# Optimization experiments

Hardware: AMD Instinct MI355X
Metric: run time of the kernel (lower is better)

The kernel has to match this reference:

```python
import jax, jax.numpy as jnp
import numpy as np

B, S, D = 4, 1024, 1024
H, DK, DV = 16, 64, 64
LN_EPS = 1e-5

def setup_inputs() -> dict:
    key = jax.random.key(0)
    ks = jax.random.split(key, 8)
    sc_q = 1.0 / np.sqrt(D)
    return {
        "Q": jax.random.normal(ks[0], (B, S, D), jnp.float32),
        "K": jax.random.normal(ks[1], (B, S, D), jnp.float32),
        "V": jax.random.normal(ks[2], (B, S, D), jnp.float32),
        "mask": jnp.zeros((B, S, S), dtype=bool),
        "W_Q": jax.random.normal(ks[3], (D, H * DK), jnp.float32) * sc_q,
        "W_K": jax.random.normal(ks[4], (D, H * DK), jnp.float32) * sc_q,
        "W_V": jax.random.normal(ks[5], (D, H * DV), jnp.float32) * sc_q,
        "W_O": jax.random.normal(ks[6], (H * DV, D), jnp.float32) * (1.0 / np.sqrt(H * DV)),
        "ln_gamma": jnp.ones((D,), jnp.float32),
        "ln_beta": jnp.zeros((D,), jnp.float32),
    }

def reference(Q, K, V, mask, W_Q, W_K, W_V, W_O, ln_gamma, ln_beta):
    residual = Q
    # projections -> [B, H, S, dk/dv]
    q = (Q @ W_Q).reshape(B, S, H, DK).transpose(0, 2, 1, 3)
    k = (K @ W_K).reshape(B, S, H, DK).transpose(0, 2, 1, 3)
    v = (V @ W_V).reshape(B, S, H, DV).transpose(0, 2, 1, 3)
    # scores [B, H, Sq, Sk]
    scores = jnp.einsum('bhqd,bhkd->bhqk', q, k) / jnp.sqrt(jnp.float32(DK))
    scores = jnp.where(mask[:, None, :, :], -jnp.inf, scores)
    # faithful to original: softmax over dim=2 (the QUERY axis)
    attn = jax.nn.softmax(scores, axis=2)
    out = jnp.einsum('bhqk,bhkd->bhqd', attn, v)  # [B, H, Sq, dv]
    out = out.transpose(0, 2, 1, 3).reshape(B, S, H * DV)
    out = out @ W_O + residual
    # LayerNorm over last dim
    mu = jnp.mean(out, axis=-1, keepdims=True)
    var = jnp.var(out, axis=-1, keepdims=True)
    out = (out - mu) * jax.lax.rsqrt(var + LN_EPS) * ln_gamma + ln_beta
    return out, attn
```

## Files before the change

### kernel.cpp

```cpp
#include <hip/hip_runtime.h>
#include <hip/hip_bf16.h>


typedef __bf16 bf16;
typedef bf16 bf16x4 __attribute__((ext_vector_type(4)));
typedef bf16 bf16x8 __attribute__((ext_vector_type(8)));
typedef float f32x4 __attribute__((ext_vector_type(4)));
typedef unsigned char u8x16 __attribute__((ext_vector_type(16)));

#define MFMA(a, b, c) __builtin_amdgcn_mfma_f32_16x16x32_bf16((a), (b), (c), 0, 0, 0)

__device__ __forceinline__ bf16 f2b(float x) { return (bf16)x; }

__device__ __forceinline__ void gl_lds16(const bf16* g, void* l) {
    __builtin_amdgcn_global_load_lds(
        (const __attribute__((address_space(1))) void*)g,
        (__attribute__((address_space(3))) void*)l, 16, 0, 0);
}

__device__ __forceinline__ void bar_lgkm() {
    __builtin_amdgcn_sched_barrier(0);
    asm volatile("s_waitcnt lgkmcnt(0)" ::: "memory");
    __builtin_amdgcn_sched_barrier(0);
    __builtin_amdgcn_s_barrier();
    __builtin_amdgcn_sched_barrier(0);
}

__global__ __launch_bounds__(256) void k_cvt(
    const float* __restrict__ Q, const float* __restrict__ K, const float* __restrict__ V,
    bf16* __restrict__ Qb, bf16* __restrict__ Kb, bf16* __restrict__ Vb)
{
    const int z = blockIdx.y;
    const float* src = z == 0 ? Q : z == 1 ? K : V;
    bf16* dst = z == 0 ? Qb : z == 1 ? Kb : Vb;
    const float sc = z == 0 ? 0.125f : 1.0f;
    size_t idx = ((size_t)blockIdx.x * 256 + threadIdx.x) * 8;
    const size_t stride = (size_t)gridDim.x * 2048;
    for (; idx < 4194304; idx += stride) {
        const float4 v0 = *(const float4*)(src + idx);
        const float4 v1 = *(const float4*)(src + idx + 4);
        bf16x8 o = { f2b(v0.x * sc), f2b(v0.y * sc), f2b(v0.z * sc), f2b(v0.w * sc),
                     f2b(v1.x * sc), f2b(v1.y * sc), f2b(v1.z * sc), f2b(v1.w * sc) };
        *(bf16x8*)(dst + idx) = o;
    }
}

__global__ __launch_bounds__(256) void k_transpose(
    const float* __restrict__ W0, const float* __restrict__ W1,
    const float* __restrict__ W2, const float* __restrict__ W3,
    bf16* __restrict__ T0, bf16* __restrict__ T1,
    bf16* __restrict__ T2, bf16* __restrict__ T3)
{
    const float* W = blockIdx.z == 0 ? W0 : blockIdx.z == 1 ? W1 : blockIdx.z == 2 ? W2 : W3;
    bf16*        T = blockIdx.z == 0 ? T0 : blockIdx.z == 1 ? T1 : blockIdx.z == 2 ? T2 : T3;
    __shared__ float tile[32][33];
    const int t = threadIdx.x;
    const int r = t >> 3, c = (t & 7) * 4;
    {
        const float4 v = *(const float4*)(W + (size_t)(blockIdx.y * 32 + r) * 1024 + blockIdx.x * 32 + c);
        tile[r][c + 0] = v.x; tile[r][c + 1] = v.y; tile[r][c + 2] = v.z; tile[r][c + 3] = v.w;
    }
    __syncthreads();
    bf16x4 o = { f2b(tile[c + 0][r]), f2b(tile[c + 1][r]), f2b(tile[c + 2][r]), f2b(tile[c + 3][r]) };
    *(bf16x4*)(T + (size_t)(blockIdx.x * 32 + r) * 1024 + blockIdx.y * 32 + c) = o;
}

__global__ __launch_bounds__(256) void k_proj(
    const bf16* __restrict__ Xq, const bf16* __restrict__ Xk, const bf16* __restrict__ Xv,
    const bf16* __restrict__ WTq, const bf16* __restrict__ WTk, const bf16* __restrict__ WTv,
    bf16* __restrict__ qh, bf16* __restrict__ kh, bf16* __restrict__ vTh)
{
    const int z = blockIdx.z;
    const bf16* X  = z == 0 ? Xq : z == 1 ? Xk : Xv;
    const bf16* WT = z == 0 ? WTq : z == 1 ? WTk : WTv;

    __shared__ char AsB[16384];
    __shared__ char BsB[16384];

    const int tid = threadIdx.x;
    const int lane = tid & 63, w = tid >> 6;
    const int lr = lane & 15, lg = lane >> 4;
    const int wm = w >> 1, wn = w & 1;
    const int m0 = blockIdx.y * 128, n0 = blockIdx.x * 128;

    const int srow = lane >> 3;
    const int swz8 = ((lane & 7) ^ srow) * 8;
    const bf16* Ab = X  + (size_t)(m0 + w * 32 + srow) * 1024 + swz8;
    const bf16* Bb = WT + (size_t)(n0 + w * 32 + srow) * 1024 + swz8;
    char* Alb = AsB + w * 4096;
    char* Blb = BsB + w * 4096;

    f32x4 acc[4][4] = {};

    for (int k0 = 0; k0 < 1024; k0 += 64) {
        #pragma unroll
        for (int i = 0; i < 4; ++i) {
            gl_lds16(Ab + (size_t)i * 8192 + k0, Alb + i * 1024);
            gl_lds16(Bb + (size_t)i * 8192 + k0, Blb + i * 1024);
        }
        __syncthreads();
        #pragma unroll
        for (int ks = 0; ks < 2; ++ks) {
            const int swr = ((ks * 4 + lg) ^ (lr & 7)) << 4;
            bf16x8 a[4], bb[4];
            #pragma unroll
            for (int fm = 0; fm < 4; ++fm)
                a[fm] = *(const bf16x8*)(AsB + (wm * 64 + fm * 16 + lr) * 128 + swr);
            #pragma unroll
            for (int fn = 0; fn < 4; ++fn)
                bb[fn] = *(const bf16x8*)(BsB + (wn * 64 + fn * 16 + lr) * 128 + swr);
            #pragma unroll
            for (int fm = 0; fm < 4; ++fm)
                #pragma unroll
                for (int fn = 0; fn < 4; ++fn)
                    acc[fm][fn] = MFMA(a[fm], bb[fn], acc[fm][fn]);
        }
        __syncthreads();
    }

    if (z < 2) {
        bf16* dst = (z == 0) ? qh : kh;
        #pragma unroll
        for (int fm = 0; fm < 4; ++fm)
            #pragma unroll
            for (int fn = 0; fn < 4; ++fn)
                #pragma unroll
                for (int r = 0; r < 4; ++r) {
                    const int m = m0 + wm * 64 + fm * 16 + lg * 4 + r;
                    const int n = n0 + wn * 64 + fn * 16 + lr;
                    const int b = m >> 10, s = m & 1023, h = n >> 6, d = n & 63;
                    dst[(((size_t)(b * 16 + h)) * 1024 + s) * 64 + d] = f2b(acc[fm][fn][r]);
                }
    } else {
        #pragma unroll
        for (int fm = 0; fm < 4; ++fm)
            #pragma unroll
            for (int fn = 0; fn < 4; ++fn) {
                const int m = m0 + wm * 64 + fm * 16 + lg * 4;
                const int n = n0 + wn * 64 + fn * 16 + lr;
                const int b = m >> 10, s = m & 1023, h = n >> 6, d = n & 63;
                bf16x4 o = { f2b(acc[fm][fn][0]), f2b(acc[fm][fn][1]),
                             f2b(acc[fm][fn][2]), f2b(acc[fm][fn][3]) };
                *(bf16x4*)&vTh[(((size_t)(b * 16 + h)) * 64 + d) * 1024 + s] = o;
            }
    }
}

__global__ __launch_bounds__(256) void k_colsum(
    const bf16* __restrict__ qh, const bf16* __restrict__ kh,
    const unsigned char* __restrict__ mask, float* __restrict__ inv_colsum)
{
    const int bh = blockIdx.y;
    const int b = bh >> 4;
    const int kk0 = blockIdx.x * 32;
    const bf16* qb = qh + (size_t)bh * 65536;
    const bf16* kb = kh + (size_t)bh * 65536;
    const unsigned char* mb = mask + (size_t)b * 1048576;

    const int tid = threadIdx.x;
    const int lane = tid & 63, w = tid >> 6;
    const int lr = lane & 15, lg = lane >> 4;

    __shared__ unsigned char Ml[2][128 * 48];
    __shared__ float csum[4][32];

    const int mrow = tid >> 1, mcoff = (tid & 1) * 16;

    bf16x8 bfr[2][2];
    #pragma unroll
    for (int fn = 0; fn < 2; ++fn)
        #pragma unroll
        for (int ks = 0; ks < 2; ++ks)
            bfr[fn][ks] = *(const bf16x8*)(kb + (size_t)(kk0 + fn * 16 + lr) * 64 + ks * 32 + lg * 8);

    *(u8x16*)&Ml[0][mrow * 48 + mcoff] =
        *(const u8x16*)(mb + (size_t)mrow * 1024 + kk0 + mcoff);
    bar_lgkm();

    float colacc[2][4] = {};

    for (int q0 = 0; q0 < 1024; q0 += 128) {
        const int cur = (q0 >> 7) & 1;
        if (q0 + 128 < 1024)
            *(u8x16*)&Ml[cur ^ 1][mrow * 48 + mcoff] =
                *(const u8x16*)(mb + (size_t)(q0 + 128 + mrow) * 1024 + kk0 + mcoff);

        #pragma unroll
        for (int fm = 0; fm < 2; ++fm) {
            const int ql = w * 32 + fm * 16 + lr;
            const int q = q0 + ql;
            const bf16x8 a0 = *(const bf16x8*)(qb + (size_t)q * 64 + lg * 8);
            const bf16x8 a1 = *(const bf16x8*)(qb + (size_t)q * 64 + 32 + lg * 8);
            #pragma unroll
            for (int fn = 0; fn < 2; ++fn) {
                f32x4 c = {0.f, 0.f, 0.f, 0.f};
                c = MFMA(bfr[fn][0], a0, c);
                c = MFMA(bfr[fn][1], a1, c);
                const unsigned int m4 = *(const unsigned int*)&Ml[cur][ql * 48 + fn * 16 + lg * 4];
                #pragma unroll
                for (int r = 0; r < 4; ++r)
                    colacc[fn][r] += ((m4 >> (8 * r)) & 255u) ? 0.f : __expf(c[r]);
            }
        }
        bar_lgkm();
    }

    #pragma unroll
    for (int fn = 0; fn < 2; ++fn)
        #pragma unroll
        for (int r = 0; r < 4; ++r) {
            float v = colacc[fn][r];
            v += __shfl_xor(v, 1);
            v += __shfl_xor(v, 2);
            v += __shfl_xor(v, 4);
            v += __shfl_xor(v, 8);
            if (lr == 0) csum[w][fn * 16 + lg * 4 + r] = v;
        }
    __syncthreads();
    if (tid < 32) {
        const float s = csum[0][tid] + csum[1][tid] + csum[2][tid] + csum[3][tid];
        inv_colsum[(size_t)bh * 1024 + kk0 + tid] = 1.0f / s;
    }
}

__global__ __launch_bounds__(256) void k_attn(
    const bf16* __restrict__ qh, const bf16* __restrict__ kh, const bf16* __restrict__ vTh,
    const unsigned char* __restrict__ mask, const float* __restrict__ inv_colsum,
    float* __restrict__ attn_out, bf16* __restrict__ attn_head)
{
    const int bh = blockIdx.y;
    const int b = bh >> 4, h = bh & 15;
    const int q0 = blockIdx.x * 32;
    const bf16* qb = qh + (size_t)bh * 65536;
    const bf16* kb = kh + (size_t)bh * 65536;
    const bf16* vb = vTh + (size_t)bh * 65536;
    const unsigned char* mb = mask + (size_t)b * 1048576 + (size_t)q0 * 1024;

    const int tid = threadIdx.x;
    const int lane = tid & 63, w = tid >> 6;
    const int lr = lane & 15, lg = lane >> 4;

    __shared__ __align__(16) char smem[17408 + 9216];
    bf16* Pl = (bf16*)smem;
    unsigned char* Ml = (unsigned char*)(smem + 17408);
    f32x4* red = (f32x4*)smem;
    bf16* Ao = (bf16*)(smem + 17408);

    const int mrow = tid >> 3, mcoff = (tid & 7) * 16;

    bf16x8 af[2][2];
    #pragma unroll
    for (int fm = 0; fm < 2; ++fm)
        #pragma unroll
        for (int ks = 0; ks < 2; ++ks)
            af[fm][ks] = *(const bf16x8*)(qb + (size_t)(q0 + fm * 16 + lr) * 64 + ks * 32 + lg * 8);

    *(u8x16*)&Ml[mrow * 144 + mcoff] = *(const u8x16*)(mb + (size_t)mrow * 1024 + mcoff);
    bar_lgkm();

    f32x4 pacc[2][4] = {};

    for (int kk0 = 0; kk0 < 1024; kk0 += 128) {
        const int cur = (kk0 >> 7) & 1;
        bf16* P = Pl + cur * 32 * 136;
        const unsigned char* Mc = Ml + cur * 32 * 144;

        if (kk0 + 128 < 1024)
            *(u8x16*)&Ml[(cur ^ 1) * 32 * 144 + mrow * 144 + mcoff] =
                *(const u8x16*)(mb + (size_t)mrow * 1024 + kk0 + 128 + mcoff);

        bf16x8 bfr[2][2];
        #pragma unroll
        for (int fn = 0; fn < 2; ++fn)
            #pragma unroll
            for (int ks = 0; ks < 2; ++ks)
                bfr[fn][ks] = *(const bf16x8*)(kb + (size_t)(kk0 + w * 32 + fn * 16 + lr) * 64 + ks * 32 + lg * 8);
        f32x4 linv[2];
        #pragma unroll
        for (int fn = 0; fn < 2; ++fn)
            linv[fn] = *(const f32x4*)(inv_colsum + (size_t)bh * 1024 + kk0 + w * 32 + fn * 16 + lg * 4);

        #pragma unroll
        for (int fm = 0; fm < 2; ++fm)
            #pragma unroll
            for (int fn = 0; fn < 2; ++fn) {
                f32x4 c = {0.f, 0.f, 0.f, 0.f};
                c = MFMA(bfr[fn][0], af[fm][0], c);
                c = MFMA(bfr[fn][1], af[fm][1], c);
                const int ql = fm * 16 + lr;
                const int kloc = w * 32 + fn * 16 + lg * 4;
                const unsigned int m4 = *(const unsigned int*)&Mc[ql * 144 + kloc];
                bf16x4 pb;
                #pragma unroll
                for (int r = 0; r < 4; ++r)
                    pb[r] = f2b(((m4 >> (8 * r)) & 255u) ? 0.f : __expf(c[r]) * linv[fn][r]);
                *(bf16x4*)&P[ql * 136 + kloc] = pb;
            }

        bar_lgkm();

        #pragma unroll
        for (int fm2 = 0; fm2 < 2; ++fm2) {
            const bf16x8 pa = *(const bf16x8*)&P[(fm2 * 16 + lr) * 136 + w * 32 + lg * 8];
            #pragma unroll
            for (int fn2 = 0; fn2 < 4; ++fn2) {
                const bf16x8 vv = *(const bf16x8*)(vb + (size_t)(fn2 * 16 + lr) * 1024 + kk0 + w * 32 + lg * 8);
                pacc[fm2][fn2] = MFMA(pa, vv, pacc[fm2][fn2]);
            }
        }

        {
            const int srow = tid >> 5;
            const int c4 = (tid & 31) * 4;
            #pragma unroll
            for (int rr = 0; rr < 4; ++rr) {
                const int row = srow + rr * 8;
                const uint2 pv = *(const uint2*)&P[row * 136 + c4];
                f32x4 o;
                o[0] = __uint_as_float(pv.x << 16);
                o[1] = __uint_as_float(pv.x & 0xffff0000u);
                o[2] = __uint_as_float(pv.y << 16);
                o[3] = __uint_as_float(pv.y & 0xffff0000u);
                *(f32x4*)(attn_out + ((size_t)bh * 1024 + q0 + row) * 1024 + kk0 + c4) = o;
            }
        }
    }

    __syncthreads();
    if (w >= 2)
        #pragma unroll
        for (int fm2 = 0; fm2 < 2; ++fm2)
            #pragma unroll
            for (int fn2 = 0; fn2 < 4; ++fn2)
                red[(fm2 * 4 + fn2) * 128 + (w - 2) * 64 + lane] = pacc[fm2][fn2];
    __syncthreads();
    if (w < 2)
        #pragma unroll
        for (int fm2 = 0; fm2 < 2; ++fm2)
            #pragma unroll
            for (int fn2 = 0; fn2 < 4; ++fn2)
                pacc[fm2][fn2] += red[(fm2 * 4 + fn2) * 128 + w * 64 + lane];
    __syncthreads();
    if (w == 1)
        #pragma unroll
        for (int fm2 = 0; fm2 < 2; ++fm2)
            #pragma unroll
            for (int fn2 = 0; fn2 < 4; ++fn2)
                red[(fm2 * 4 + fn2) * 128 + lane] = pacc[fm2][fn2];
    __syncthreads();
    if (w == 0)
        #pragma unroll
        for (int fm2 = 0; fm2 < 2; ++fm2)
            #pragma unroll
            for (int fn2 = 0; fn2 < 4; ++fn2) {
                const f32x4 s = pacc[fm2][fn2] + red[(fm2 * 4 + fn2) * 128 + lane];
                #pragma unroll
                for (int r = 0; r < 4; ++r)
                    Ao[(fm2 * 16 + lg * 4 + r) * 72 + fn2 * 16 + lr] = f2b(s[r]);
            }
    __syncthreads();
    {
        const int row = tid >> 3, c8 = (tid & 7) * 8;
        const bf16x8 v = *(const bf16x8*)&Ao[row * 72 + c8];
        *(bf16x8*)(attn_head + ((size_t)b * 1024 + q0 + row) * 1024 + h * 64 + c8) = v;
    }
}

__global__ __launch_bounds__(256) void k_outproj(
    const bf16* __restrict__ Ah, const bf16* __restrict__ WTo,
    const float* __restrict__ Qres, float* __restrict__ proj)
{
    __shared__ char AsB[16384];
    __shared__ char BsB[16384];

    const int tid = threadIdx.x;
    const int lane = tid & 63, w = tid >> 6;
    const int lr = lane & 15, lg = lane >> 4;
    const int wm = w >> 1, wn = w & 1;
    const int m0 = blockIdx.y * 128, n0 = blockIdx.x * 128;

    const int srow = lane >> 3;
    const int swz8 = ((lane & 7) ^ srow) * 8;
    const bf16* Ab = Ah  + (size_t)(m0 + w * 32 + srow) * 1024 + swz8;
    const bf16* Bb = WTo + (size_t)(n0 + w * 32 + srow) * 1024 + swz8;
    char* Alb = AsB + w * 4096;
    char* Blb = BsB + w * 4096;

    f32x4 acc[4][4] = {};

    for (int k0 = 0; k0 < 1024; k0 += 64) {
        #pragma unroll
        for (int i = 0; i < 4; ++i) {
            gl_lds16(Ab + (size_t)i * 8192 + k0, Alb + i * 1024);
            gl_lds16(Bb + (size_t)i * 8192 + k0, Blb + i * 1024);
        }
        __syncthreads();
        #pragma unroll
        for (int ks = 0; ks < 2; ++ks) {
            const int swr = ((ks * 4 + lg) ^ (lr & 7)) << 4;
            bf16x8 a[4], bb[4];
            #pragma unroll
            for (int fm = 0; fm < 4; ++fm)
                a[fm] = *(const bf16x8*)(AsB + (wm * 64 + fm * 16 + lr) * 128 + swr);
            #pragma unroll
            for (int fn = 0; fn < 4; ++fn)
                bb[fn] = *(const bf16x8*)(BsB + (wn * 64 + fn * 16 + lr) * 128 + swr);
            #pragma unroll
            for (int fm = 0; fm < 4; ++fm)
                #pragma unroll
                for (int fn = 0; fn < 4; ++fn)
                    acc[fm][fn] = MFMA(a[fm], bb[fn], acc[fm][fn]);
        }
        __syncthreads();
    }

    #pragma unroll
    for (int fm = 0; fm < 4; ++fm)
        #pragma unroll
        for (int fn = 0; fn < 4; ++fn)
            #pragma unroll
            for (int r = 0; r < 4; ++r) {
                const int m = m0 + wm * 64 + fm * 16 + lg * 4 + r;
                const int n = n0 + wn * 64 + fn * 16 + lr;
                proj[(size_t)m * 1024 + n] = acc[fm][fn][r] + Qres[(size_t)m * 1024 + n];
            }
}

__global__ __launch_bounds__(256) void k_ln(
    const float* __restrict__ proj, const float* __restrict__ gam,
    const float* __restrict__ bet, float* __restrict__ out)
{
    const int row = blockIdx.x;
    const int t = threadIdx.x;
    const int lane = t & 63, w = t >> 6;
    const float4 x = *(const float4*)(proj + (size_t)row * 1024 + t * 4);
    float s = x.x + x.y + x.z + x.w;
    float ss = x.x * x.x + x.y * x.y + x.z * x.z + x.w * x.w;
    #pragma unroll
    for (int o = 1; o < 64; o <<= 1) {
        s += __shfl_xor(s, o);
        ss += __shfl_xor(ss, o);
    }
    __shared__ float rs[4], rss[4];
    if (lane == 0) { rs[w] = s; rss[w] = ss; }
    __syncthreads();
    const float S1 = rs[0] + rs[1] + rs[2] + rs[3];
    const float S2 = rss[0] + rss[1] + rss[2] + rss[3];
    const float mu = S1 * (1.0f / 1024.0f);
    const float rstd = rsqrtf(S2 * (1.0f / 1024.0f) - mu * mu + 1e-5f);
    const float4 gg = *(const float4*)(gam + t * 4);
    const float4 bb = *(const float4*)(bet + t * 4);
    float4 y;
    y.x = (x.x - mu) * rstd * gg.x + bb.x;
    y.y = (x.y - mu) * rstd * gg.y + bb.y;
    y.z = (x.z - mu) * rstd * gg.z + bb.z;
    y.w = (x.w - mu) * rstd * gg.w + bb.w;
    *(float4*)(out + (size_t)row * 1024 + t * 4) = y;
}

extern "C" void kernel_launch(void* const* d_in, const int* in_sizes, int n_in,
                              void* d_out, int out_size, void* d_ws, size_t ws_size,
                              hipStream_t stream)
{
    const float* Q  = (const float*)d_in[0];
    const float* K  = (const float*)d_in[1];
    const float* V  = (const float*)d_in[2];
    const unsigned char* mask = (const unsigned char*)d_in[3];
    const float* W_Q = (const float*)d_in[4];
    const float* W_K = (const float*)d_in[5];
    const float* W_V = (const float*)d_in[6];
    const float* W_O = (const float*)d_in[7];
    const float* gam = (const float*)d_in[8];
    const float* bet = (const float*)d_in[9];

    float* out  = (float*)d_out;
    float* attn = out + (size_t)4 * 1024 * 1024;

    bf16* wsb = (bf16*)d_ws;
    const size_t M1 = 1024 * 1024;
    bf16* WTq = wsb + 0 * M1;
    bf16* WTk = wsb + 1 * M1;
    bf16* WTv = wsb + 2 * M1;
    bf16* WTo = wsb + 3 * M1;
    bf16* qh  = wsb + 4 * M1;
    bf16* kh  = wsb + 8 * M1;
    bf16* vTh = wsb + 12 * M1;
    bf16* Xqb = wsb + 16 * M1;
    bf16* Xkb = wsb + 20 * M1;
    bf16* Xvb = wsb + 24 * M1;
    bf16* Ah  = wsb + 16 * M1;
    float* inv_colsum = (float*)(wsb + 20 * M1);
    float* proj       = inv_colsum + 65536;

    const dim3 blk(256);
    k_cvt<<<dim3(512, 3), blk, 0, stream>>>(Q, K, V, Xqb, Xkb, Xvb);
    k_transpose<<<dim3(32, 32, 4), blk, 0, stream>>>(W_Q, W_K, W_V, W_O, WTq, WTk, WTv, WTo);
    k_proj<<<dim3(8, 32, 3), blk, 0, stream>>>(Xqb, Xkb, Xvb, WTq, WTk, WTv, qh, kh, vTh);
    k_colsum<<<dim3(32, 64), blk, 0, stream>>>(qh, kh, mask, inv_colsum);
    k_attn<<<dim3(32, 64), blk, 0, stream>>>(qh, kh, vTh, mask, inv_colsum, attn, Ah);
    k_outproj<<<dim3(8, 32), blk, 0, stream>>>(Ah, WTo, Q, proj);
    k_ln<<<dim3(4096), blk, 0, stream>>>(proj, gam, bet, out);
}
```

Measured before the change: 255.7 us.

## Halve GEMM M-tile to 64 and remap attention blocks for XCD locality

The projection and output-projection GEMMs move from 128x128 to 64x128 tiles. This doubles the grid (1536 and 512 blocks) so the many CUs are better filled, and it cuts LDS and accumulator use per block. The colsum and attention kernels switch to a 1D grid with a bid&7 remap so that consecutive workgroups of the same head land on the same XCD, improving L2 reuse of K/V. In exchange, the smaller tiles lower arithmetic intensity and reload more of the B operand.

```diff
diff --git a/kernel.cpp b/kernel.cpp
--- a/kernel.cpp
+++ b/kernel.cpp
@@ -74,43 +74,43 @@
     const bf16* X  = z == 0 ? Xq : z == 1 ? Xk : Xv;
     const bf16* WT = z == 0 ? WTq : z == 1 ? WTk : WTv;
 
-    __shared__ char AsB[16384];
+    __shared__ char AsB[8192];
     __shared__ char BsB[16384];
 
     const int tid = threadIdx.x;
     const int lane = tid & 63, w = tid >> 6;
     const int lr = lane & 15, lg = lane >> 4;
     const int wm = w >> 1, wn = w & 1;
-    const int m0 = blockIdx.y * 128, n0 = blockIdx.x * 128;
-
-    const int srow = lane >> 3;
-    const int swz8 = ((lane & 7) ^ srow) * 8;
-    const bf16* Ab = X  + (size_t)(m0 + w * 32 + srow) * 1024 + swz8;
-    const bf16* Bb = WT + (size_t)(n0 + w * 32 + srow) * 1024 + swz8;
-    char* Alb = AsB + w * 4096;
-    char* Blb = BsB + w * 4096;
-
-    f32x4 acc[4][4] = {};
+    const int m0 = blockIdx.y * 64, n0 = blockIdx.x * 128;
+
+    const int lrow = lane >> 3;
+    const int swz8 = ((lane & 7) ^ lrow) * 8;
+    const bf16* Ab = X  + (size_t)(m0 + w * 8 + lrow) * 1024 + swz8;
+    const bf16* Bb = WT + (size_t)(n0 + w * 8 + lrow) * 1024 + swz8;
+    char* Alb = AsB + w * 1024;
+    char* Blb = BsB + w * 1024;
+
+    f32x4 acc[2][4] = {};
 
     for (int k0 = 0; k0 < 1024; k0 += 64) {
-        #pragma unroll
-        for (int i = 0; i < 4; ++i) {
-            gl_lds16(Ab + (size_t)i * 8192 + k0, Alb + i * 1024);
-            gl_lds16(Bb + (size_t)i * 8192 + k0, Blb + i * 1024);
-        }
+        gl_lds16(Ab + k0,          Alb);
+        gl_lds16(Ab + 32768 + k0,  Alb + 4096);
+        #pragma unroll
+        for (int i = 0; i < 4; ++i)
+            gl_lds16(Bb + (size_t)i * 32768 + k0, Blb + i * 4096);
         __syncthreads();
         #pragma unroll
         for (int ks = 0; ks < 2; ++ks) {
             const int swr = ((ks * 4 + lg) ^ (lr & 7)) << 4;
-            bf16x8 a[4], bb[4];
-            #pragma unroll
-            for (int fm = 0; fm < 4; ++fm)
-                a[fm] = *(const bf16x8*)(AsB + (wm * 64 + fm * 16 + lr) * 128 + swr);
+            bf16x8 a[2], bb[4];
+            #pragma unroll
+            for (int fm = 0; fm < 2; ++fm)
+                a[fm] = *(const bf16x8*)(AsB + (wm * 32 + fm * 16 + lr) * 128 + swr);
             #pragma unroll
             for (int fn = 0; fn < 4; ++fn)
                 bb[fn] = *(const bf16x8*)(BsB + (wn * 64 + fn * 16 + lr) * 128 + swr);
             #pragma unroll
-            for (int fm = 0; fm < 4; ++fm)
+            for (int fm = 0; fm < 2; ++fm)
                 #pragma unroll
                 for (int fn = 0; fn < 4; ++fn)
                     acc[fm][fn] = MFMA(a[fm], bb[fn], acc[fm][fn]);
@@ -121,22 +121,22 @@
     if (z < 2) {
         bf16* dst = (z == 0) ? qh : kh;
         #pragma unroll
-        for (int fm = 0; fm < 4; ++fm)
+        for (int fm = 0; fm < 2; ++fm)
             #pragma unroll
             for (int fn = 0; fn < 4; ++fn)
                 #pragma unroll
                 for (int r = 0; r < 4; ++r) {
-                    const int m = m0 + wm * 64 + fm * 16 + lg * 4 + r;
+                    const int m = m0 + wm * 32 + fm * 16 + lg * 4 + r;
                     const int n = n0 + wn * 64 + fn * 16 + lr;
                     const int b = m >> 10, s = m & 1023, h = n >> 6, d = n & 63;
                     dst[(((size_t)(b * 16 + h)) * 1024 + s) * 64 + d] = f2b(acc[fm][fn][r]);
                 }
     } else {
         #pragma unroll
-        for (int fm = 0; fm < 4; ++fm)
+        for (int fm = 0; fm < 2; ++fm)
             #pragma unroll
             for (int fn = 0; fn < 4; ++fn) {
-                const int m = m0 + wm * 64 + fm * 16 + lg * 4;
+                const int m = m0 + wm * 32 + fm * 16 + lg * 4;
                 const int n = n0 + wn * 64 + fn * 16 + lr;
                 const int b = m >> 10, s = m & 1023, h = n >> 6, d = n & 63;
                 bf16x4 o = { f2b(acc[fm][fn][0]), f2b(acc[fm][fn][1]),
@@ -150,9 +150,11 @@
     const bf16* __restrict__ qh, const bf16* __restrict__ kh,
     const unsigned char* __restrict__ mask, float* __restrict__ inv_colsum)
 {
-    const int bh = blockIdx.y;
+    const int bid = blockIdx.x;
+    const int wg = (bid & 7) * 256 + (bid >> 3);
+    const int bh = wg >> 5;
+    const int kk0 = (wg & 31) * 32;
     const int b = bh >> 4;
-    const int kk0 = blockIdx.x * 32;
     const bf16* qb = qh + (size_t)bh * 65536;
     const bf16* kb = kh + (size_t)bh * 65536;
     const unsigned char* mb = mask + (size_t)b * 1048576;
@@ -228,9 +230,11 @@
     const unsigned char* __restrict__ mask, const float* __restrict__ inv_colsum,
     float* __restrict__ attn_out, bf16* __restrict__ attn_head)
 {
-    const int bh = blockIdx.y;
+    const int bid = blockIdx.x;
+    const int wg = (bid & 7) * 256 + (bid >> 3);
+    const int bh = wg >> 5;
+    const int q0 = (wg & 31) * 32;
     const int b = bh >> 4, h = bh & 15;
-    const int q0 = blockIdx.x * 32;
     const bf16* qb = qh + (size_t)bh * 65536;
     const bf16* kb = kh + (size_t)bh * 65536;
     const bf16* vb = vTh + (size_t)bh * 65536;
@@ -370,43 +374,43 @@
     const bf16* __restrict__ Ah, const bf16* __restrict__ WTo,
     const float* __restrict__ Qres, float* __restrict__ proj)
 {
-    __shared__ char AsB[16384];
+    __shared__ char AsB[8192];
     __shared__ char BsB[16384];
 
     const int tid = threadIdx.x;
     const int lane = tid & 63, w = tid >> 6;
     const int lr = lane & 15, lg = lane >> 4;
     const int wm = w >> 1, wn = w & 1;
-    const int m0 = blockIdx.y * 128, n0 = blockIdx.x * 128;
-
-    const int srow = lane >> 3;
-    const int swz8 = ((lane & 7) ^ srow) * 8;
-    const bf16* Ab = Ah  + (size_t)(m0 + w * 32 + srow) * 1024 + swz8;
-    const bf16* Bb = WTo + (size_t)(n0 + w * 32 + srow) * 1024 + swz8;
-    char* Alb = AsB + w * 4096;
-    char* Blb = BsB + w * 4096;
-
-    f32x4 acc[4][4] = {};
+    const int m0 = blockIdx.y * 64, n0 = blockIdx.x * 128;
+
+    const int lrow = lane >> 3;
+    const int swz8 = ((lane & 7) ^ lrow) * 8;
+    const bf16* Ab = Ah  + (size_t)(m0 + w * 8 + lrow) * 1024 + swz8;
+    const bf16* Bb = WTo + (size_t)(n0 + w * 8 + lrow) * 1024 + swz8;
+    char* Alb = AsB + w * 1024;
+    char* Blb = BsB + w * 1024;
+
+    f32x4 acc[2][4] = {};
 
     for (int k0 = 0; k0 < 1024; k0 += 64) {
-        #pragma unroll
-        for (int i = 0; i < 4; ++i) {
-            gl_lds16(Ab + (size_t)i * 8192 + k0, Alb + i * 1024);
-            gl_lds16(Bb + (size_t)i * 8192 + k0, Blb + i * 1024);
-        }
+        gl_lds16(Ab + k0,         Alb);
+        gl_lds16(Ab + 32768 + k0, Alb + 4096);
+        #pragma unroll
+        for (int i = 0; i < 4; ++i)
+            gl_lds16(Bb + (size_t)i * 32768 + k0, Blb + i * 4096);
         __syncthreads();
         #pragma unroll
         for (int ks = 0; ks < 2; ++ks) {
             const int swr = ((ks * 4 + lg) ^ (lr & 7)) << 4;
-            bf16x8 a[4], bb[4];
-            #pragma unroll
-            for (int fm = 0; fm < 4; ++fm)
-                a[fm] = *(const bf16x8*)(AsB + (wm * 64 + fm * 16 + lr) * 128 + swr);
+            bf16x8 a[2], bb[4];
+            #pragma unroll
+            for (int fm = 0; fm < 2; ++fm)
+                a[fm] = *(const bf16x8*)(AsB + (wm * 32 + fm * 16 + lr) * 128 + swr);
             #pragma unroll
             for (int fn = 0; fn < 4; ++fn)
                 bb[fn] = *(const bf16x8*)(BsB + (wn * 64 + fn * 16 + lr) * 128 + swr);
             #pragma unroll
-            for (int fm = 0; fm < 4; ++fm)
+            for (int fm = 0; fm < 2; ++fm)
                 #pragma unroll
                 for (int fn = 0; fn < 4; ++fn)
                     acc[fm][fn] = MFMA(a[fm], bb[fn], acc[fm][fn]);
@@ -415,12 +419,12 @@
     }
 
     #pragma unroll
-    for (int fm = 0; fm < 4; ++fm)
+    for (int fm = 0; fm < 2; ++fm)
         #pragma unroll
         for (int fn = 0; fn < 4; ++fn)
             #pragma unroll
             for (int r = 0; r < 4; ++r) {
-                const int m = m0 + wm * 64 + fm * 16 + lg * 4 + r;
+                const int m = m0 + wm * 32 + fm * 16 + lg * 4 + r;
                 const int n = n0 + wn * 64 + fn * 16 + lr;
                 proj[(size_t)m * 1024 + n] = acc[fm][fn][r] + Qres[(size_t)m * 1024 + n];
             }
@@ -495,9 +499,9 @@
     const dim3 blk(256);
     k_cvt<<<dim3(512, 3), blk, 0, stream>>>(Q, K, V, Xqb, Xkb, Xvb);
     k_transpose<<<dim3(32, 32, 4), blk, 0, stream>>>(W_Q, W_K, W_V, W_O, WTq, WTk, WTv, WTo);
-    k_proj<<<dim3(8, 32, 3), blk, 0, stream>>>(Xqb, Xkb, Xvb, WTq, WTk, WTv, qh, kh, vTh);
-    k_colsum<<<dim3(32, 64), blk, 0, stream>>>(qh, kh, mask, inv_colsum);
-    k_attn<<<dim3(32, 64), blk, 0, stream>>>(qh, kh, vTh, mask, inv_colsum, attn, Ah);
-    k_outproj<<<dim3(8, 32), blk, 0, stream>>>(Ah, WTo, Q, proj);
+    k_proj<<<dim3(8, 64, 3), blk, 0, stream>>>(Xqb, Xkb, Xvb, WTq, WTk, WTv, qh, kh, vTh);
+    k_colsum<<<dim3(2048), blk, 0, stream>>>(qh, kh, mask, inv_colsum);
+    k_attn<<<dim3(2048), blk, 0, stream>>>(qh, kh, vTh, mask, inv_colsum, attn, Ah);
+    k_outproj<<<dim3(8, 64), blk, 0, stream>>>(Ah, WTo, Q, proj);
     k_ln<<<dim3(4096), blk, 0, stream>>>(proj, gam, bet, out);
 }
```

Result: faster. 244.9 us (-4.2%).
